# Kernel optimization log

Hardware: AMD Instinct MI355X
Metric: run time of the kernel (lower is better)

The kernel has to match this reference:

```python
import jax, jax.numpy as jnp
import numpy as np

T, H, I, E, K = 2048, 1024, 768, 16, 4

def setup_inputs() -> dict:
    key = jax.random.key(0)
    k1, k2, k3, k4, k5 = jax.random.split(key, 5)
    hidden_states = jax.random.normal(k1, (T, H), dtype=jnp.float32)
    top_k_index = jax.random.randint(k2, (T, K), 0, E, dtype=jnp.int64)
    top_k_weights = jax.random.uniform(k3, (T, K), dtype=jnp.float32)
    gate_up_proj = jax.random.normal(k4, (E, 2 * I, H), dtype=jnp.float32) * 0.02
    down_proj = jax.random.normal(k5, (E, H, I), dtype=jnp.float32) * 0.02
    return {"hidden_states": hidden_states, "top_k_index": top_k_index,
            "top_k_weights": top_k_weights, "gate_up_proj": gate_up_proj,
            "down_proj": down_proj}

def reference(hidden_states, top_k_index, top_k_weights, gate_up_proj, down_proj):
    # Masked dense MoE: scan over experts, each expert does full-token GEMMs
    # and a per-token combine weight (sum of routing weights where routed to e).
    # index_add over token_idx == sum over k of (mask * weight) * expert_out.
    n_experts = gate_up_proj.shape[0]

    def body(acc, xs):
        w_gu, w_d, e = xs  # [2I,H], [H,I], scalar
        gu = hidden_states @ w_gu.T                 # [T, 2I]
        gate, up = jnp.split(gu, 2, axis=-1)        # [T, I] each
        h = jax.nn.silu(gate) * up                  # [T, I]
        out = h @ w_d.T                             # [T, H]
        w_tok = jnp.sum(jnp.where(top_k_index == e, top_k_weights, 0.0), axis=-1)  # [T]
        return acc + out * w_tok[:, None], None

    acc0 = jnp.zeros_like(hidden_states)
    final, _ = jax.lax.scan(body, acc0, (gate_up_proj, down_proj, jnp.arange(n_experts)))
    return final
```

## Files before the change

### kernel.cpp

```cpp
#include <hip/hip_runtime.h>
#include <hip/hip_bf16.h>
#include <stdint.h>

#define T_TOK 2048
#define H_DIM 1024
#define I_DIM 768
#define E_NUM 16
#define K_TOP 4
#define NSLOT (T_TOK * K_TOP)
#define PSLOT 10240
#define NTILE 80

typedef short  s16x8 __attribute__((ext_vector_type(8)));
typedef float  f32x4 __attribute__((ext_vector_type(4)));
typedef unsigned short u16x8 __attribute__((ext_vector_type(8)));
typedef unsigned int   u32x4 __attribute__((ext_vector_type(4)));

#define MEMFENCE asm volatile("" ::: "memory")

__device__ __forceinline__ void gload16(const void* g, void* l) {
  __builtin_amdgcn_global_load_lds(
      (const __attribute__((address_space(1))) uint32_t*)g,
      (__attribute__((address_space(3))) uint32_t*)l, 16, 0, 0);
}

__device__ __forceinline__ unsigned short f2bf(float f) {
  __hip_bfloat16 h = __float2bfloat16(f);
  return *reinterpret_cast<unsigned short*>(&h);
}

__device__ __forceinline__ unsigned int cvtpk(float lo, float hi) {
  unsigned int r;
  asm("v_cvt_pk_bf16_f32 %0, %1, %2" : "=v"(r) : "v"(lo), "v"(hi));
  return r;
}

__device__ __forceinline__ void write_b_row(char* bregion, int r, int half,
                                            f32x4 f0, f32x4 f1, f32x4 f2, f32x4 f3) {
  union { u32x4 u; u16x8 s; } a_, b_;
  a_.u[0] = cvtpk(f0[0], f0[1]); a_.u[1] = cvtpk(f0[2], f0[3]);
  a_.u[2] = cvtpk(f1[0], f1[1]); a_.u[3] = cvtpk(f1[2], f1[3]);
  b_.u[0] = cvtpk(f2[0], f2[1]); b_.u[1] = cvtpk(f2[2], f2[3]);
  b_.u[2] = cvtpk(f3[0], f3[1]); b_.u[3] = cvtpk(f3[2], f3[3]);
  int xr = (r >> 1) & 3;
  char* wb = bregion + r * 64;
  *(u16x8*)(wb + (((2*half + 0) ^ xr) * 16)) = a_.s;
  *(u16x8*)(wb + (((2*half + 1) ^ xr) * 16)) = b_.s;
}

__global__ __launch_bounds__(256) void cvt_bf16_kernel(
    const float* __restrict__ in, unsigned short* __restrict__ out, int n8) {
  int i = blockIdx.x * 256 + threadIdx.x;
  if (i >= n8) return;
  const float4* p = (const float4*)in;
  float4 a = p[2 * (size_t)i];
  float4 b = p[2 * (size_t)i + 1];
  u16x8 o;
  o[0] = f2bf(a.x); o[1] = f2bf(a.y); o[2] = f2bf(a.z); o[3] = f2bf(a.w);
  o[4] = f2bf(b.x); o[5] = f2bf(b.y); o[6] = f2bf(b.z); o[7] = f2bf(b.w);
  *(u16x8*)(out + (size_t)i * 8) = o;
}

__global__ __launch_bounds__(256) void route_kernel(
    const int* __restrict__ idx, const float* __restrict__ wts,
    int* __restrict__ slot_tok, float* __restrict__ slot_w,
    int* __restrict__ slot_of, int* __restrict__ tile_expert) {
  __shared__ int cnt[256][16];
  __shared__ int tot[16];
  __shared__ int pb[17];
  int tid = threadIdx.x;

  for (int e = 0; e < 16; ++e) cnt[tid][e] = 0;
  const int s0 = tid * 32;
  for (int i = 0; i < 32; ++i) {
    int e = idx[s0 + i] & 15;
    cnt[tid][e]++;
  }
  __syncthreads();
  if (tid < 16) {
    int run = 0;
    for (int c = 0; c < 256; ++c) { int v = cnt[c][tid]; cnt[c][tid] = run; run += v; }
    tot[tid] = run;
  }
  __syncthreads();
  if (tid == 0) {
    int acc = 0;
    for (int e = 0; e < 16; ++e) { pb[e] = acc; acc += (tot[e] + 127) & ~127; }
    pb[16] = acc;
  }
  __syncthreads();
  for (int p = tid; p < PSLOT; p += 256) { slot_tok[p] = 0; slot_w[p] = 0.0f; }
  if (tid < NTILE) {
    int ef = -1;
    for (int e = 0; e < 16; ++e)
      if (tid * 128 >= pb[e] && tid * 128 < pb[e + 1]) ef = e;
    tile_expert[tid] = ef;
  }
  __syncthreads();
  for (int i = 0; i < 32; ++i) {
    int s = s0 + i;
    int e = idx[s] & 15;
    int pos = pb[e] + cnt[tid][e]++;
    slot_tok[pos] = s >> 2;
    slot_w[pos]   = wts[s];
    slot_of[s]    = pos;
  }
}

__global__ __launch_bounds__(256) void gemm1_kernel(
    const unsigned short* __restrict__ Xbf,
    const float* __restrict__ Wgu,
    const int* __restrict__ slot_tok,
    const int* __restrict__ tile_expert,
    unsigned short* __restrict__ hbuf) {
  int bid  = blockIdx.y * 12 + blockIdx.x;
  int sbid = (bid & 7) * 120 + (bid >> 3);
  int by   = sbid / 12;
  int bx   = sbid % 12;
  int e = tile_expert[by];
  if (e < 0) return;
  int m0 = by * 128;
  int t = threadIdx.x;
  int lane = t & 63, w = t >> 6;
  int wr = w >> 1, wc = w & 1;
  int l15 = lane & 15, lhi = lane >> 4;

  __shared__ char lds[2 * 24576];
  char* buf0 = lds;
  char* buf1 = lds + 24576;

  int arow = t >> 2;
  int aswz = ((t & 3) ^ ((t >> 3) & 3)) * 16;
  int tok0 = slot_tok[m0 + arow];
  int tok1 = slot_tok[m0 + 64 + arow];
  const char* gA0 = (const char*)(Xbf + (size_t)tok0 * H_DIM) + aswz;
  const char* gA1 = (const char*)(Xbf + (size_t)tok1 * H_DIM) + aswz;

  const char* gBs[4];
#pragma unroll
  for (int c = 0; c < 4; ++c) {
    int r = c * 32 + (t >> 3);
    int prow = (r < 64) ? (bx * 64 + r) : (768 + bx * 64 + (r - 64));
    int q = (t & 7) ^ (r & 7);
    gBs[c] = (const char*)(Wgu + ((size_t)e * 1536 + prow) * H_DIM) + q * 16;
  }

  int pswz = (lhi ^ ((l15 >> 1) & 3)) * 8;

  f32x4 accg[4][2] = {};
  f32x4 accu[4][2] = {};

#define NT1 32
#define G1_STAGE(bufp, kt) do {                               \
    size_t ao = (size_t)(kt) * 64;                            \
    size_t bo = (size_t)(kt) * 128;                           \
    gload16(gA0 + ao, (bufp) + t * 16);                       \
    gload16(gA1 + ao, (bufp) + 4096 + t * 16);                \
    gload16(gBs[0] + bo, (bufp) + 8192 + t * 16);             \
    gload16(gBs[1] + bo, (bufp) + 12288 + t * 16);            \
    gload16(gBs[2] + bo, (bufp) + 16384 + t * 16);            \
    gload16(gBs[3] + bo, (bufp) + 20480 + t * 16);            \
  } while (0)

#define B_FRAG(dst, cb, rb) do {                                              \
    const char* base_ = (cb) + 8192 + (rb) * 128;                             \
    f32x4 x0_ = *(const f32x4*)(base_ + (((2*lhi    ) ^ ((rb) & 7)) * 16));   \
    f32x4 x1_ = *(const f32x4*)(base_ + (((2*lhi + 1) ^ ((rb) & 7)) * 16));   \
    union { u32x4 u; s16x8 s; } pk_;                                          \
    pk_.u[0] = cvtpk(x0_[0], x0_[1]);                                         \
    pk_.u[1] = cvtpk(x0_[2], x0_[3]);                                         \
    pk_.u[2] = cvtpk(x1_[0], x1_[1]);                                         \
    pk_.u[3] = cvtpk(x1_[2], x1_[3]);                                         \
    dst = pk_.s;                                                              \
  } while (0)

#define G1_COMPUTE(cb) do {                                                            \
    const short* La = (const short*)(cb);                                              \
    s16x8 af[4], bg[2], bu[2];                                                         \
    _Pragma("unroll")                                                                  \
    for (int mi = 0; mi < 4; ++mi)                                                     \
      af[mi] = *(const s16x8*)(La + (wr * 64 + mi * 16 + l15) * 32 + pswz);            \
    _Pragma("unroll")                                                                  \
    for (int ni = 0; ni < 2; ++ni) {                                                   \
      int rbg = wc * 32 + ni * 16 + l15;                                               \
      B_FRAG(bg[ni], (cb), rbg);                                                       \
      B_FRAG(bu[ni], (cb), rbg + 64);                                                  \
    }                                                                                  \
    __builtin_amdgcn_s_setprio(1);                                                     \
    _Pragma("unroll")                                                                  \
    for (int mi = 0; mi < 4; ++mi)                                                     \
      _Pragma("unroll")                                                                \
      for (int ni = 0; ni < 2; ++ni) {                                                 \
        accg[mi][ni] = __builtin_amdgcn_mfma_f32_16x16x32_bf16(af[mi], bg[ni], accg[mi][ni], 0, 0, 0); \
        accu[mi][ni] = __builtin_amdgcn_mfma_f32_16x16x32_bf16(af[mi], bu[ni], accu[mi][ni], 0, 0, 0); \
      }                                                                                \
    __builtin_amdgcn_s_setprio(0);                                                     \
  } while (0)

  G1_STAGE(buf0, 0);
  int cur = 0;
  for (int kt = 0; kt < NT1; ++kt) {
    char* cbuf = cur ? buf1 : buf0;
    char* nbuf = cur ? buf0 : buf1;
    if (kt + 1 < NT1) {
      MEMFENCE;
      G1_STAGE(nbuf, kt + 1);
      asm volatile("s_waitcnt vmcnt(6)" ::: "memory");
    } else {
      asm volatile("s_waitcnt vmcnt(0)" ::: "memory");
    }
    __builtin_amdgcn_s_barrier();
    MEMFENCE;
    G1_COMPUTE(cbuf);
    MEMFENCE;
    __builtin_amdgcn_s_barrier();
    cur ^= 1;
  }
#undef G1_STAGE
#undef G1_COMPUTE
#undef B_FRAG

#pragma unroll
  for (int mi = 0; mi < 4; ++mi) {
#pragma unroll
    for (int ni = 0; ni < 2; ++ni) {
      int col = bx * 64 + wc * 32 + ni * 16 + l15;
#pragma unroll
      for (int q = 0; q < 4; ++q) {
        int m = m0 + wr * 64 + mi * 16 + lhi * 4 + q;
        float g = accg[mi][ni][q];
        float u = accu[mi][ni][q];
        float s = g / (1.0f + __expf(-g));
        hbuf[(size_t)m * I_DIM + col] = f2bf(s * u);
      }
    }
  }
}

__global__ __launch_bounds__(256) void gemm2_kernel(
    const unsigned short* __restrict__ hbuf,
    const float* __restrict__ Wd,
    const int* __restrict__ slot_tok,
    const float* __restrict__ slot_w,
    const int* __restrict__ tile_expert,
    float* __restrict__ y) {
  int bid  = blockIdx.y * 8 + blockIdx.x;
  int sbid = (bid & 7) * 80 + (bid >> 3);
  int by   = sbid >> 3;
  int bx   = sbid & 7;
  int e = tile_expert[by];
  if (e < 0) return;
  int m0 = by * 128;
  int tid = threadIdx.x;
  int lane = tid & 63, w = tid >> 6;
  int wr = w >> 1, wc = w & 1;

  __shared__ short lds[2 * 8192];
  char* buf0 = (char*)lds;
  char* buf1 = buf0 + 16384;

  int srow = tid >> 2;
  int swzc = ((tid & 3) ^ ((tid >> 3) & 3)) * 16;
  const char* gA0 = (const char*)(hbuf + (size_t)(m0 + srow) * I_DIM) + swzc;
  const char* gA1 = (const char*)(hbuf + (size_t)(m0 + 64 + srow) * I_DIM) + swzc;

  int brow = tid >> 1;
  int half = tid & 1;
  const float* gB = Wd + ((size_t)e * 1024 + bx * 128 + brow) * I_DIM + half * 16;

  int pswz = ((lane >> 4) ^ (((lane & 15) >> 1) & 3)) * 8;

  f32x4 acc[4][4] = {};
  f32x4 s0_0, s0_1, s0_2, s0_3, s1_0, s1_1, s1_2, s1_3;
  f32x4 s2_0, s2_1, s2_2, s2_3, s3_0, s3_1, s3_2, s3_3;

#define NT2 24
#define A_GLOAD2(kt, bufp) do {                               \
    int kk_ = (kt) < NT2 ? (kt) : NT2 - 1;                    \
    int ko_ = kk_ * 64;                                       \
    gload16(gA0 + ko_, (bufp) + tid * 16);                    \
    gload16(gA1 + ko_, (bufp) + 4096 + tid * 16);             \
  } while (0)
#define B_LOAD2(v0, v1, v2, v3, kt) do {                      \
    int kk_ = (kt) < NT2 ? (kt) : NT2 - 1;                    \
    const f32x4* p_ = (const f32x4*)(gB + (size_t)kk_ * 32);  \
    v0 = p_[0]; v1 = p_[1]; v2 = p_[2]; v3 = p_[3];           \
  } while (0)

#define G2_COMPUTE(bufp) do {                                                          \
    const short* La = (const short*)(bufp);                                            \
    s16x8 af[4], bf[4];                                                                \
    _Pragma("unroll")                                                                  \
    for (int mi = 0; mi < 4; ++mi)                                                     \
      af[mi] = *(const s16x8*)(La + (wr * 64 + mi * 16 + (lane & 15)) * 32 + pswz);    \
    _Pragma("unroll")                                                                  \
    for (int ni = 0; ni < 4; ++ni)                                                     \
      bf[ni] = *(const s16x8*)(La + 4096 + (wc * 64 + ni * 16 + (lane & 15)) * 32 + pswz); \
    _Pragma("unroll")                                                                  \
    for (int mi = 0; mi < 4; ++mi)                                                     \
      _Pragma("unroll")                                                                \
      for (int ni = 0; ni < 4; ++ni)                                                   \
        acc[mi][ni] = __builtin_amdgcn_mfma_f32_16x16x32_bf16(af[mi], bf[ni], acc[mi][ni], 0, 0, 0); \
  } while (0)

#define ITER2(kt, wv0, wv1, wv2, wv3, lv0, lv1, lv2, lv3) do {  \
    char* cbuf_ = ((kt) & 1) ? buf1 : buf0;                     \
    char* nbuf_ = ((kt) & 1) ? buf0 : buf1;                     \
    MEMFENCE;                                                   \
    A_GLOAD2((kt) + 1, nbuf_);                                  \
    MEMFENCE;                                                   \
    B_LOAD2(lv0, lv1, lv2, lv3, (kt) + 3);                      \
    asm volatile("s_waitcnt vmcnt(10)" ::: "memory");           \
    write_b_row(nbuf_ + 8192, brow, half, wv0, wv1, wv2, wv3);  \
    asm volatile("s_waitcnt lgkmcnt(0)" ::: "memory");          \
    __builtin_amdgcn_s_barrier();                               \
    MEMFENCE;                                                   \
    G2_COMPUTE(cbuf_);                                          \
    MEMFENCE;                                                   \
    __builtin_amdgcn_s_barrier();                               \
  } while (0)

  A_GLOAD2(0, buf0);
  MEMFENCE;
  B_LOAD2(s0_0, s0_1, s0_2, s0_3, 0);
  MEMFENCE;
  B_LOAD2(s1_0, s1_1, s1_2, s1_3, 1);
  MEMFENCE;
  B_LOAD2(s2_0, s2_1, s2_2, s2_3, 2);
  asm volatile("s_waitcnt vmcnt(8)" ::: "memory");
  write_b_row(buf0 + 8192, brow, half, s0_0, s0_1, s0_2, s0_3);

  for (int kt = 0; kt < NT2; kt += 4) {
    ITER2(kt + 0, s1_0, s1_1, s1_2, s1_3, s3_0, s3_1, s3_2, s3_3);
    ITER2(kt + 1, s2_0, s2_1, s2_2, s2_3, s0_0, s0_1, s0_2, s0_3);
    ITER2(kt + 2, s3_0, s3_1, s3_2, s3_3, s1_0, s1_1, s1_2, s1_3);
    ITER2(kt + 3, s0_0, s0_1, s0_2, s0_3, s2_0, s2_1, s2_2, s2_3);
  }
#undef ITER2
#undef G2_COMPUTE
#undef B_LOAD2
#undef A_GLOAD2

#pragma unroll
  for (int mi = 0; mi < 4; ++mi) {
#pragma unroll
    for (int q = 0; q < 4; ++q) {
      int m = m0 + wr * 64 + mi * 16 + (lane >> 4) * 4 + q;
      float wgt = slot_w[m];
      float* orow = y + (size_t)m * H_DIM + bx * 128 + wc * 64 + (lane & 15);
#pragma unroll
      for (int ni = 0; ni < 4; ++ni)
        orow[ni * 16] = acc[mi][ni][q] * wgt;
    }
  }
}

__global__ __launch_bounds__(256) void combine_kernel(
    const float* __restrict__ y, const int* __restrict__ slot_of,
    float* __restrict__ out) {
  int t = blockIdx.x;
  int c = threadIdx.x * 4;
  int s0 = slot_of[t * 4 + 0], s1 = slot_of[t * 4 + 1];
  int s2 = slot_of[t * 4 + 2], s3 = slot_of[t * 4 + 3];
  f32x4 v0 = *(const f32x4*)(y + (size_t)s0 * H_DIM + c);
  f32x4 v1 = *(const f32x4*)(y + (size_t)s1 * H_DIM + c);
  f32x4 v2 = *(const f32x4*)(y + (size_t)s2 * H_DIM + c);
  f32x4 v3 = *(const f32x4*)(y + (size_t)s3 * H_DIM + c);
  f32x4 r = (v0 + v1) + (v2 + v3);
  *(f32x4*)(out + (size_t)t * H_DIM + c) = r;
}

extern "C" void kernel_launch(void* const* d_in, const int* in_sizes, int n_in,
                              void* d_out, int out_size, void* d_ws, size_t ws_size,
                              hipStream_t stream) {
  const float* hs       = (const float*)d_in[0];
  const int*   topk_idx = (const int*)d_in[1];
  const float* topk_w   = (const float*)d_in[2];
  const float* w_gu     = (const float*)d_in[3];
  const float* w_d      = (const float*)d_in[4];
  float* out = (float*)d_out;

  char* ws = (char*)d_ws;
  unsigned short* Xbf  = (unsigned short*)(ws);
  unsigned short* hbuf = (unsigned short*)(ws + 4194304);
  float*          y    = (float*)(ws + 19922944);
  int*   slot_tok    = (int*)(ws + 61865984);
  float* slot_w      = (float*)(ws + 61906944);
  int*   slot_of     = (int*)(ws + 61947904);
  int*   tile_expert = (int*)(ws + 61980672);

  cvt_bf16_kernel<<<1024, 256, 0, stream>>>(hs, Xbf, T_TOK * H_DIM / 8);
  route_kernel<<<1, 256, 0, stream>>>(topk_idx, topk_w, slot_tok, slot_w,
                                      slot_of, tile_expert);

  gemm1_kernel<<<dim3(12, NTILE), 256, 0, stream>>>(Xbf, w_gu, slot_tok, tile_expert, hbuf);
  gemm2_kernel<<<dim3(8, NTILE), 256, 0, stream>>>(hbuf, w_d, slot_tok, slot_w, tile_expert, y);
  combine_kernel<<<T_TOK, 256, 0, stream>>>(y, slot_of, out);
}
```

Before: 129.2 us.

## Enlarge gemm1 M-tile to 256 rows with 512-thread blocks

Pads each expert's token slots to multiples of 256 and runs gate/up GEMM with 256-row tiles on 512-thread blocks (8 waves). Each fp32 weight tile is loaded once per 256 tokens instead of per 128, halving redundant weight traffic in gemm1. gemm2 keeps 128-row tiles via a separate tile map. The cost is more padding waste (up to 255 slots per expert), fewer gemm1 blocks, and larger LDS use per block.

```diff
diff --git a/kernel.cpp b/kernel.cpp
--- a/kernel.cpp
+++ b/kernel.cpp
@@ -7,9 +7,10 @@
 #define I_DIM 768
 #define E_NUM 16
 #define K_TOP 4
-#define NSLOT (T_TOK * K_TOP)
-#define PSLOT 10240
-#define NTILE 80
+#define NSLOT 8192
+#define PSLOT 12288
+#define NT256 48
+#define NT128 96
 
 typedef short  s16x8 __attribute__((ext_vector_type(8)));
 typedef float  f32x4 __attribute__((ext_vector_type(4)));
@@ -64,7 +65,8 @@
 __global__ __launch_bounds__(256) void route_kernel(
     const int* __restrict__ idx, const float* __restrict__ wts,
     int* __restrict__ slot_tok, float* __restrict__ slot_w,
-    int* __restrict__ slot_of, int* __restrict__ tile_expert) {
+    int* __restrict__ slot_of, int* __restrict__ tile_expert,
+    int* __restrict__ tile_expert128) {
   __shared__ int cnt[256][16];
   __shared__ int tot[16];
   __shared__ int pb[17];
@@ -85,16 +87,23 @@
   __syncthreads();
   if (tid == 0) {
     int acc = 0;
-    for (int e = 0; e < 16; ++e) { pb[e] = acc; acc += (tot[e] + 127) & ~127; }
+    for (int e = 0; e < 16; ++e) { pb[e] = acc; acc += (tot[e] + 255) & ~255; }
     pb[16] = acc;
   }
   __syncthreads();
   for (int p = tid; p < PSLOT; p += 256) { slot_tok[p] = 0; slot_w[p] = 0.0f; }
-  if (tid < NTILE) {
+  if (tid < NT256) {
     int ef = -1;
     for (int e = 0; e < 16; ++e)
-      if (tid * 128 >= pb[e] && tid * 128 < pb[e + 1]) ef = e;
+      if (tid * 256 >= pb[e] && tid * 256 < pb[e + 1]) ef = e;
     tile_expert[tid] = ef;
+  }
+  if (tid >= 64 && tid < 64 + NT128) {
+    int m = (tid - 64) * 128;
+    int ef = -1;
+    for (int e = 0; e < 16; ++e)
+      if (m >= pb[e] && m < pb[e + 1]) ef = e;
+    tile_expert128[tid - 64] = ef;
   }
   __syncthreads();
   for (int i = 0; i < 32; ++i) {
@@ -107,43 +116,38 @@
   }
 }
 
-__global__ __launch_bounds__(256) void gemm1_kernel(
+__global__ __launch_bounds__(512) void gemm1_kernel(
     const unsigned short* __restrict__ Xbf,
     const float* __restrict__ Wgu,
     const int* __restrict__ slot_tok,
     const int* __restrict__ tile_expert,
     unsigned short* __restrict__ hbuf) {
   int bid  = blockIdx.y * 12 + blockIdx.x;
-  int sbid = (bid & 7) * 120 + (bid >> 3);
+  int sbid = (bid & 7) * 72 + (bid >> 3);
   int by   = sbid / 12;
   int bx   = sbid % 12;
   int e = tile_expert[by];
   if (e < 0) return;
-  int m0 = by * 128;
+  int m0 = by * 256;
   int t = threadIdx.x;
   int lane = t & 63, w = t >> 6;
   int wr = w >> 1, wc = w & 1;
   int l15 = lane & 15, lhi = lane >> 4;
 
-  __shared__ char lds[2 * 24576];
+  __shared__ char lds[2 * 32768];
   char* buf0 = lds;
-  char* buf1 = lds + 24576;
-
-  int arow = t >> 2;
+  char* buf1 = lds + 32768;
+
   int aswz = ((t & 3) ^ ((t >> 3) & 3)) * 16;
-  int tok0 = slot_tok[m0 + arow];
-  int tok1 = slot_tok[m0 + 64 + arow];
-  const char* gA0 = (const char*)(Xbf + (size_t)tok0 * H_DIM) + aswz;
-  const char* gA1 = (const char*)(Xbf + (size_t)tok1 * H_DIM) + aswz;
-
-  const char* gBs[4];
-#pragma unroll
-  for (int c = 0; c < 4; ++c) {
-    int r = c * 32 + (t >> 3);
-    int prow = (r < 64) ? (bx * 64 + r) : (768 + bx * 64 + (r - 64));
-    int q = (t & 7) ^ (r & 7);
-    gBs[c] = (const char*)(Wgu + ((size_t)e * 1536 + prow) * H_DIM) + q * 16;
-  }
+  int tokA0 = slot_tok[m0 + (t >> 2)];
+  int tokA1 = slot_tok[m0 + 128 + (t >> 2)];
+  const char* gA0 = (const char*)(Xbf + (size_t)tokA0 * H_DIM) + aswz;
+  const char* gA1 = (const char*)(Xbf + (size_t)tokA1 * H_DIM) + aswz;
+
+  int brq = (t & 7) ^ ((t >> 3) & 7);
+  int br  = t >> 3;
+  const char* gB0 = (const char*)(Wgu + ((size_t)e * 1536 + bx * 64 + br) * H_DIM) + brq * 16;
+  const char* gB1 = (const char*)(Wgu + ((size_t)e * 1536 + 768 + bx * 64 + br) * H_DIM) + brq * 16;
 
   int pswz = (lhi ^ ((l15 >> 1) & 3)) * 8;
 
@@ -155,15 +159,13 @@
     size_t ao = (size_t)(kt) * 64;                            \
     size_t bo = (size_t)(kt) * 128;                           \
     gload16(gA0 + ao, (bufp) + t * 16);                       \
-    gload16(gA1 + ao, (bufp) + 4096 + t * 16);                \
-    gload16(gBs[0] + bo, (bufp) + 8192 + t * 16);             \
-    gload16(gBs[1] + bo, (bufp) + 12288 + t * 16);            \
-    gload16(gBs[2] + bo, (bufp) + 16384 + t * 16);            \
-    gload16(gBs[3] + bo, (bufp) + 20480 + t * 16);            \
+    gload16(gA1 + ao, (bufp) + 8192 + t * 16);                \
+    gload16(gB0 + bo, (bufp) + 16384 + t * 16);               \
+    gload16(gB1 + bo, (bufp) + 24576 + t * 16);               \
   } while (0)
 
 #define B_FRAG(dst, cb, rb) do {                                              \
-    const char* base_ = (cb) + 8192 + (rb) * 128;                             \
+    const char* base_ = (cb) + 16384 + (rb) * 128;                            \
     f32x4 x0_ = *(const f32x4*)(base_ + (((2*lhi    ) ^ ((rb) & 7)) * 16));   \
     f32x4 x1_ = *(const f32x4*)(base_ + (((2*lhi + 1) ^ ((rb) & 7)) * 16));   \
     union { u32x4 u; s16x8 s; } pk_;                                          \
@@ -205,7 +207,7 @@
     if (kt + 1 < NT1) {
       MEMFENCE;
       G1_STAGE(nbuf, kt + 1);
-      asm volatile("s_waitcnt vmcnt(6)" ::: "memory");
+      asm volatile("s_waitcnt vmcnt(4)" ::: "memory");
     } else {
       asm volatile("s_waitcnt vmcnt(0)" ::: "memory");
     }
@@ -242,13 +244,13 @@
     const float* __restrict__ Wd,
     const int* __restrict__ slot_tok,
     const float* __restrict__ slot_w,
-    const int* __restrict__ tile_expert,
+    const int* __restrict__ tile_expert128,
     float* __restrict__ y) {
   int bid  = blockIdx.y * 8 + blockIdx.x;
-  int sbid = (bid & 7) * 80 + (bid >> 3);
+  int sbid = (bid & 7) * 96 + (bid >> 3);
   int by   = sbid >> 3;
   int bx   = sbid & 7;
-  int e = tile_expert[by];
+  int e = tile_expert128[by];
   if (e < 0) return;
   int m0 = by * 128;
   int tid = threadIdx.x;
@@ -383,17 +385,18 @@
   char* ws = (char*)d_ws;
   unsigned short* Xbf  = (unsigned short*)(ws);
   unsigned short* hbuf = (unsigned short*)(ws + 4194304);
-  float*          y    = (float*)(ws + 19922944);
-  int*   slot_tok    = (int*)(ws + 61865984);
-  float* slot_w      = (float*)(ws + 61906944);
-  int*   slot_of     = (int*)(ws + 61947904);
-  int*   tile_expert = (int*)(ws + 61980672);
+  float*          y    = (float*)(ws + 23068672);
+  int*   slot_tok       = (int*)(ws + 73400320);
+  float* slot_w         = (float*)(ws + 73449472);
+  int*   slot_of        = (int*)(ws + 73498624);
+  int*   tile_expert    = (int*)(ws + 73531392);
+  int*   tile_expert128 = (int*)(ws + 73531648);
 
   cvt_bf16_kernel<<<1024, 256, 0, stream>>>(hs, Xbf, T_TOK * H_DIM / 8);
   route_kernel<<<1, 256, 0, stream>>>(topk_idx, topk_w, slot_tok, slot_w,
-                                      slot_of, tile_expert);
-
-  gemm1_kernel<<<dim3(12, NTILE), 256, 0, stream>>>(Xbf, w_gu, slot_tok, tile_expert, hbuf);
-  gemm2_kernel<<<dim3(8, NTILE), 256, 0, stream>>>(hbuf, w_d, slot_tok, slot_w, tile_expert, y);
+                                      slot_of, tile_expert, tile_expert128);
+
+  gemm1_kernel<<<dim3(12, NT256), 512, 0, stream>>>(Xbf, w_gu, slot_tok, tile_expert, hbuf);
+  gemm2_kernel<<<dim3(8, NT128), 256, 0, stream>>>(hbuf, w_d, slot_tok, slot_w, tile_expert128, y);
   combine_kernel<<<T_TOK, 256, 0, stream>>>(y, slot_of, out);
 }
```

Measured after the change: 135.9 us. 1.05x slower.
